# Performance work log

Hardware: AMD Instinct MI355X
Metric: run time of the kernel (lower is better)

Reference implementation:

```python
import jax, jax.numpy as jnp
import numpy as np

B, L = 16384, 200
N_USERS, N_ITEMS, N_CATS, N_DUR = 1_000_000, 100_000, 1000, 50
UD, ID, CD, DD, SD = 64, 64, 16, 8, 64
UDENSE, IDENSE = 25, 3
CONCAT = UD + ID + CD + DD + UDENSE + IDENSE + SD  # 244
NE, EH, EO, NT = 8, 256, 128, 2
T1, T2 = 64, 32  # tower dims
AH1, AH2 = 64, 16  # DIN attention hidden dims
NEG_INF = -1e9


def setup_inputs() -> dict:
    key = jax.random.key(0)
    ks = iter(jax.random.split(key, 40))
    nrm = lambda shape, s: jax.random.normal(next(ks), shape, jnp.float32) * s
    inp = {
        'user_id': jax.random.randint(next(ks), (B,), 0, N_USERS),
        'item_id': jax.random.randint(next(ks), (B,), 0, N_ITEMS),
        'item_category': jax.random.randint(next(ks), (B,), 0, N_CATS),
        'item_dur_bkt': jax.random.randint(next(ks), (B,), 0, N_DUR),
        'user_dense': jax.random.normal(next(ks), (B, UDENSE), jnp.float32),
        'item_dense': jax.random.normal(next(ks), (B, IDENSE), jnp.float32),
        'history_seq': jax.random.randint(next(ks), (B, L), 0, N_ITEMS + 1),
    }
    # embeddings (std=0.01 as in _init_weights); hist row 0 is padding_idx -> zero
    inp['user_E'] = nrm((N_USERS, UD), 0.01)
    inp['item_E'] = nrm((N_ITEMS, ID), 0.01)
    inp['cat_E'] = nrm((N_CATS, CD), 0.01)
    inp['dur_E'] = nrm((N_DUR, DD), 0.01)
    inp['hist_E'] = nrm((N_ITEMS + 1, SD), 0.01).at[0].set(0.0)
    inp['Wproj'] = nrm((ID, SD), 0.12)  # xavier-ish for target_proj (no bias)
    # DIN attention MLP: 4*SD -> 64 -> 16 -> 1
    inp['aW1'] = nrm((4 * SD, AH1), 0.06); inp['ab1'] = jnp.zeros((AH1,), jnp.float32)
    inp['aW2'] = nrm((AH1, AH2), 0.15);    inp['ab2'] = jnp.zeros((AH2,), jnp.float32)
    inp['aW3'] = nrm((AH2, 1), 0.3);       inp['ab3'] = jnp.zeros((1,), jnp.float32)
    # stacked experts: concat -> 256 -> 128 (ReLU both)
    inp['eW1'] = nrm((NE, CONCAT, EH), 0.06); inp['eb1'] = jnp.zeros((NE, EH), jnp.float32)
    inp['eW2'] = nrm((NE, EH, EO), 0.06);     inp['eb2'] = jnp.zeros((NE, EO), jnp.float32)
    # per-task gates: concat -> NE softmax
    inp['gW'] = nrm((NT, CONCAT, NE), 0.06); inp['gb'] = jnp.zeros((NT, NE), jnp.float32)
    # stacked towers: 128 -> 64 -> 32 -> 1
    inp['tW1'] = nrm((NT, EO, T1), 0.09); inp['tb1'] = jnp.zeros((NT, T1), jnp.float32)
    inp['tW2'] = nrm((NT, T1, T2), 0.12); inp['tb2'] = jnp.zeros((NT, T2), jnp.float32)
    inp['tW3'] = nrm((NT, T2, 1), 0.17);  inp['tb3'] = jnp.zeros((NT, 1), jnp.float32)
    return inp


def reference(user_id, item_id, item_category, item_dur_bkt, user_dense, item_dense,
              history_seq, user_E, item_E, cat_E, dur_E, hist_E, Wproj,
              aW1, ab1, aW2, ab2, aW3, ab3,
              eW1, eb1, eW2, eb2, gW, gb,
              tW1, tb1, tW2, tb2, tW3, tb3):
    # --- feature encoding ---
    i_emb = item_E[item_id]            # (B, ID)
    u_emb = user_E[user_id]            # (B, UD)
    c_emb = cat_E[item_category]       # (B, CD)
    d_emb = dur_E[item_dur_bkt]        # (B, DD)
    h_emb = hist_E[history_seq]        # (B, L, SD)
    tgt = (i_emb @ Wproj)[:, None, :]  # (B, 1, SD)
    t = jnp.broadcast_to(tgt, h_emb.shape)
    # DIN attention features: [target, hist, target-hist, target*hist]
    feat = jnp.concatenate([t, h_emb, t - h_emb, t * h_emb], axis=-1)  # (B, L, 4*SD)
    h = jax.nn.relu(feat @ aW1 + ab1)
    h = jax.nn.relu(h @ aW2 + ab2)
    scores = (h @ aW3 + ab3)[..., 0]   # (B, L)
    scores = jnp.where(history_seq == 0, NEG_INF, scores)
    attn = jax.nn.softmax(scores, axis=-1)
    pooled = jnp.einsum('bl,bld->bd', attn, h_emb)  # (B, SD)
    shared = jnp.concatenate([u_emb, i_emb, c_emb, d_emb, user_dense, item_dense, pooled], axis=-1)  # (B, CONCAT)
    # --- experts (batched GEMM) ---
    eh = jax.nn.relu(jnp.einsum('bc,ech->beh', shared, eW1) + eb1)
    eo = jax.nn.relu(jnp.einsum('beh,eho->beo', eh, eW2) + eb2)  # (B, NE, EO)
    # --- per-task gating + towers ---
    gate = jax.nn.softmax(jnp.einsum('bc,tce->bte', shared, gW) + gb, axis=-1)  # (B, T, NE)
    ti = jnp.einsum('bte,beo->bto', gate, eo)  # (B, T, EO)
    x = jax.nn.relu(jnp.einsum('bto,toh->bth', ti, tW1) + tb1)
    x = jax.nn.relu(jnp.einsum('bth,thk->btk', x, tW2) + tb2)
    logit = (jnp.einsum('btk,tkj->btj', x, tW3) + tb3)[..., 0]  # (B, T)
    pred = jax.nn.sigmoid(logit)
    return pred[:, 0], pred[:, 1]
```

## Files before the change

### kernel.cpp

```cpp
#include <hip/hip_runtime.h>
#include <hip/hip_bf16.h>
#include <cstdint>
#include <cmath>


typedef __attribute__((ext_vector_type(8))) short bfrag;
typedef __attribute__((ext_vector_type(4))) float f32x4;

__device__ __forceinline__ unsigned short f2bf(float f) {
  __hip_bfloat16 h = __float2bfloat16(f);
  return __builtin_bit_cast(unsigned short, h);
}
__device__ __forceinline__ float bf2f(unsigned short b) {
  union { unsigned u; float f; } v; v.u = ((unsigned)b) << 16;
  return v.f;
}
__device__ __forceinline__ float bfLo(unsigned hv) {
  union { unsigned u; float f; } v; v.u = hv << 16;
  return v.f;
}
__device__ __forceinline__ float bfHi(unsigned hv) {
  union { unsigned u; float f; } v; v.u = hv & 0xffff0000u;
  return v.f;
}

#define SWZ(row, col) ((col) ^ (((row) & 7) << 3))

static constexpr size_t WS_ATTNB = 0;
static constexpr size_t WS_AW2T  = WS_ATTNB + 16384;
static constexpr size_t WS_A13   = WS_AW2T + 2048;
static constexpr size_t WS_EW1T  = WS_A13 + 16384;
static constexpr size_t WS_EW2T  = WS_EW1T + 1048576;
static constexpr size_t WS_HISTB = WS_EW2T + 524288;
static constexpr size_t WS_TGT   = WS_HISTB + 12800256;
static constexpr size_t WS_TA    = WS_TGT + 2097152;
static constexpr size_t WS_SHP   = WS_TA + 4194304;
static constexpr size_t WS_EO    = WS_SHP + 8388608;
static constexpr size_t WS_GWB   = WS_EO + 33554432;
static constexpr size_t WS_TW1B  = WS_GWB + 8192;
static constexpr size_t WS_TW2B  = WS_TW1B + 32768;
static constexpr size_t WS_WPB   = WS_TW2B + 8192;
static constexpr size_t WS_WAB   = WS_WPB + 8192;

__launch_bounds__(256)
__global__ void k0_prep(const float* __restrict__ aW1, const float* __restrict__ aW2,
                        const float* __restrict__ eW1, const float* __restrict__ eW2,
                        const float* __restrict__ hist_E,
                        const float* __restrict__ gW, const float* __restrict__ tW1,
                        const float* __restrict__ tW2, const float* __restrict__ Wproj,
                        unsigned short* __restrict__ attnBt, unsigned short* __restrict__ aW2t,
                        unsigned short* __restrict__ eW1t, unsigned short* __restrict__ eW2t,
                        unsigned short* __restrict__ hist_b,
                        unsigned short* __restrict__ gWb, unsigned short* __restrict__ tW1b,
                        unsigned short* __restrict__ tW2b,
                        unsigned short* __restrict__ Wpb, unsigned short* __restrict__ WAb) {
  int tid = blockIdx.x * blockDim.x + threadIdx.x;
  int nth = gridDim.x * blockDim.x;
  for (int i = tid; i < 64 * 128; i += nth) {
    int n = i >> 7, k = i & 127;
    float v = (k < 64) ? (aW1[(64 + k) * 64 + n] - aW1[(128 + k) * 64 + n])
                       : aW1[(128 + k) * 64 + n];
    attnBt[i] = f2bf(v);
  }
  for (int i = tid; i < 16 * 64; i += nth) {
    int n = i >> 6, k = i & 63;
    aW2t[i] = f2bf(aW2[k * 16 + n]);
  }
  for (int i = tid; i < 64 * 64; i += nth) {
    int n = i >> 6, k = i & 63;
    Wpb[i] = f2bf(Wproj[k * 64 + n]);
  }
  for (int i = tid; i < 64 * 64; i += nth) {
    int n = i >> 6, k = i & 63;
    float s = 0.f;
    for (int j = 0; j < 64; ++j)
      s += Wproj[k * 64 + j] * (aW1[j * 64 + n] + aW1[(128 + j) * 64 + n]);
    WAb[i] = f2bf(s);
  }
  for (int i = tid; i < 8 * 256 * 256; i += nth) {
    int e = i >> 16, n = (i >> 8) & 255, k = i & 255;
    eW1t[i] = (k < 244) ? f2bf(eW1[(e * 244 + k) * 256 + n]) : (unsigned short)0;
  }
  for (int i = tid; i < 8 * 128 * 256; i += nth) {
    int e = i >> 15, n = (i >> 8) & 127, k = i & 255;
    eW2t[i] = f2bf(eW2[(e * 256 + k) * 128 + n]);
  }
  for (int i = tid; i < 16 * 256; i += nth) {
    int n = i >> 8, k = i & 255, t = n >> 3, e = n & 7;
    gWb[i] = (k < 244) ? f2bf(gW[(t * 244 + k) * 8 + e]) : (unsigned short)0;
  }
  for (int i = tid; i < 2 * 64 * 128; i += nth) {
    int t = i >> 13, n = (i >> 7) & 63, k = i & 127;
    tW1b[i] = f2bf(tW1[(t * 128 + k) * 64 + n]);
  }
  for (int i = tid; i < 2 * 32 * 64; i += nth) {
    int t = i >> 11, n = (i >> 6) & 31, k = i & 63;
    tW2b[i] = f2bf(tW2[(t * 64 + k) * 32 + n]);
  }
  for (int i = tid; i < 100001 * 64; i += nth) hist_b[i] = f2bf(hist_E[i]);
}

__launch_bounds__(256)
__global__ void k1_tgt(const int* __restrict__ item_id, const float* __restrict__ item_E,
                       const unsigned short* __restrict__ Wpb, const unsigned short* __restrict__ WAb,
                       const float* __restrict__ ab1,
                       unsigned short* __restrict__ tgt, float* __restrict__ tA) {
  int tid = threadIdx.x, w = tid >> 6, lane = tid & 63;
  int lr = lane & 15, g = lane >> 4;
  int b0 = blockIdx.x * 64 + w * 16;
  int iid = item_id[b0 + lr];
  bfrag ia[2];
#pragma unroll
  for (int kk = 0; kk < 2; ++kk) {
    const float* src = item_E + (size_t)iid * 64 + kk * 32 + g * 8;
    float4 x = *(const float4*)src;
    float4 y = *(const float4*)(src + 4);
    bfrag r;
    r[0] = (short)f2bf(x.x); r[1] = (short)f2bf(x.y);
    r[2] = (short)f2bf(x.z); r[3] = (short)f2bf(x.w);
    r[4] = (short)f2bf(y.x); r[5] = (short)f2bf(y.y);
    r[6] = (short)f2bf(y.z); r[7] = (short)f2bf(y.w);
    ia[kk] = r;
  }
  f32x4 at[4], aa[4];
#pragma unroll
  for (int i = 0; i < 4; ++i) { at[i] = (f32x4){0,0,0,0}; aa[i] = (f32x4){0,0,0,0}; }
#pragma unroll
  for (int kk = 0; kk < 2; ++kk)
#pragma unroll
    for (int nt = 0; nt < 4; ++nt) {
      bfrag wp = *(const bfrag*)(Wpb + (nt * 16 + lr) * 64 + kk * 32 + g * 8);
      at[nt] = __builtin_amdgcn_mfma_f32_16x16x32_bf16(ia[kk], wp, at[nt], 0, 0, 0);
      bfrag wa = *(const bfrag*)(WAb + (nt * 16 + lr) * 64 + kk * 32 + g * 8);
      aa[nt] = __builtin_amdgcn_mfma_f32_16x16x32_bf16(ia[kk], wa, aa[nt], 0, 0, 0);
    }
#pragma unroll
  for (int nt = 0; nt < 4; ++nt) {
    int n = nt * 16 + lr;
    float b1 = ab1[n];
#pragma unroll
    for (int r = 0; r < 4; ++r) {
      int m = b0 + g * 4 + r;
      tgt[(size_t)m * 64 + n] = f2bf(at[nt][r]);
      tA[(size_t)m * 64 + n] = aa[nt][r] + b1;
    }
  }
}

__launch_bounds__(256)
__global__ void k3a_assemble(const int* __restrict__ user_id, const int* __restrict__ item_id,
                             const int* __restrict__ item_cat, const int* __restrict__ item_dur,
                             const float* __restrict__ user_dense, const float* __restrict__ item_dense,
                             const float* __restrict__ user_E, const float* __restrict__ item_E,
                             const float* __restrict__ cat_E, const float* __restrict__ dur_E,
                             unsigned short* __restrict__ shared_p) {
  int tid = threadIdx.x, w = tid >> 6, lane = tid & 63;
  int b = blockIdx.x * 4 + w;
  unsigned short* row = shared_p + (size_t)b * 256;
  row[lane]      = f2bf(user_E[(size_t)user_id[b] * 64 + lane]);
  row[64 + lane] = f2bf(item_E[(size_t)item_id[b] * 64 + lane]);
  if (lane < 16) row[128 + lane] = f2bf(cat_E[item_cat[b] * 16 + lane]);
  if (lane < 8)  row[144 + lane] = f2bf(dur_E[item_dur[b] * 8 + lane]);
  if (lane < 25) row[152 + lane] = f2bf(user_dense[b * 25 + lane]);
  if (lane < 3)  row[177 + lane] = f2bf(item_dense[b * 3 + lane]);
  if (lane < 12) row[244 + lane] = 0;
}

__launch_bounds__(256, 5)
__global__ void k2_attn(const int* __restrict__ hist_seq, const unsigned short* __restrict__ hist_b,
                        const unsigned short* __restrict__ tgt, const float* __restrict__ tA,
                        const unsigned short* __restrict__ attnBt_g, const unsigned short* __restrict__ aW2t_g,
                        const float* __restrict__ ab2, const float* __restrict__ aW3,
                        unsigned short* __restrict__ shared_p) {
  __shared__ unsigned short sH1[208 * 64];
  __shared__ int   ids[208];
  __shared__ float tv[64], tAv[64];
  __shared__ float sSc[208];
  __shared__ float red[8];
  __shared__ float pbuf[512];
  int b = blockIdx.x;
  int tid = threadIdx.x, w = tid >> 6, lane = tid & 63;
  int lr = lane & 15, g = lane >> 4;

  if (tid < 208) ids[tid] = (tid < 200) ? hist_seq[(size_t)b * 200 + tid] : 0;
  if (tid < 64) tv[tid] = bf2f(tgt[(size_t)b * 64 + tid]);
  else if (tid < 128) tAv[tid - 64] = tA[(size_t)b * 64 + (tid - 64)];

  bfrag b2fr[2];
#pragma unroll
  for (int kk = 0; kk < 2; ++kk)
    b2fr[kk] = *(const bfrag*)(aW2t_g + lr * 64 + kk * 32 + g * 8);
  f32x4 ab2v4 = *(const f32x4*)(ab2 + g * 4);
  f32x4 aW3v4 = *(const f32x4*)(aW3 + g * 4);
  __syncthreads();

  {
    int n = tid >> 2, k0 = (tid & 3) * 16;
    const unsigned short* rowp = attnBt_g + n * 128;
    unsigned short a23[16], a4[16], mo[16];
    *(uint4*)(a23)     = *(const uint4*)(rowp + k0);
    *(uint4*)(a23 + 8) = *(const uint4*)(rowp + k0 + 8);
    *(uint4*)(a4)      = *(const uint4*)(rowp + 64 + k0);
    *(uint4*)(a4 + 8)  = *(const uint4*)(rowp + 64 + k0 + 8);
#pragma unroll
    for (int i = 0; i < 16; ++i)
      mo[i] = f2bf(bf2f(a23[i]) + tv[k0 + i] * bf2f(a4[i]));
    *(uint4*)(sH1 + n * 64 + SWZ(n, k0))     = *(uint4*)(mo);
    *(uint4*)(sH1 + n * 64 + SWZ(n, k0 + 8)) = *(uint4*)(mo + 8);
  }
  __syncthreads();

  bfrag mfr[4][2];
#pragma unroll
  for (int nt = 0; nt < 4; ++nt)
#pragma unroll
    for (int kk = 0; kk < 2; ++kk) {
      int n = nt * 16 + lr;
      mfr[nt][kk] = *(const bfrag*)(sH1 + n * 64 + SWZ(n, kk * 32 + g * 8));
    }
  __syncthreads();

  for (int mt = w; mt < 13; mt += 4) {
    int m = mt * 16 + lr;
    const unsigned short* hrow = hist_b + (size_t)ids[m] * 64;
    bfrag h0 = *(const bfrag*)(hrow + g * 8);
    bfrag h1 = *(const bfrag*)(hrow + 32 + g * 8);
    f32x4 acc[4] = {{0,0,0,0},{0,0,0,0},{0,0,0,0},{0,0,0,0}};
#pragma unroll
    for (int nt = 0; nt < 4; ++nt) {
      acc[nt] = __builtin_amdgcn_mfma_f32_16x16x32_bf16(mfr[nt][0], h0, acc[nt], 0, 0, 0);
      acc[nt] = __builtin_amdgcn_mfma_f32_16x16x32_bf16(mfr[nt][1], h1, acc[nt], 0, 0, 0);
    }
#pragma unroll
    for (int nt = 0; nt < 4; ++nt) {
      f32x4 ta4 = *(const f32x4*)(tAv + nt * 16 + g * 4);
      unsigned lo = (unsigned)f2bf(fmaxf(acc[nt][0] + ta4[0], 0.f))
                  | ((unsigned)f2bf(fmaxf(acc[nt][1] + ta4[1], 0.f)) << 16);
      unsigned hi = (unsigned)f2bf(fmaxf(acc[nt][2] + ta4[2], 0.f))
                  | ((unsigned)f2bf(fmaxf(acc[nt][3] + ta4[3], 0.f)) << 16);
      uint2 pk; pk.x = lo; pk.y = hi;
      *(uint2*)(sH1 + m * 64 + SWZ(m, nt * 16 + g * 4)) = pk;
    }
  }
  __syncthreads();

  for (int mt = w; mt < 13; mt += 4) {
    int m = mt * 16 + lr;
    f32x4 acc2 = {0.f, 0.f, 0.f, 0.f};
#pragma unroll
    for (int kk = 0; kk < 2; ++kk) {
      bfrag hb = *(const bfrag*)(sH1 + m * 64 + SWZ(m, kk * 32 + g * 8));
      acc2 = __builtin_amdgcn_mfma_f32_16x16x32_bf16(b2fr[kk], hb, acc2, 0, 0, 0);
    }
    float p = 0.f;
#pragma unroll
    for (int r = 0; r < 4; ++r)
      p += fmaxf(acc2[r] + ab2v4[r], 0.f) * aW3v4[r];
    p += __shfl_xor(p, 16);
    p += __shfl_xor(p, 32);
    if (lane < 16) sSc[m] = p;
  }
  __syncthreads();

  bool valid = false; float sc0 = 0.f;
  if (tid < 200 && ids[tid] != 0) { valid = true; sc0 = sSc[tid]; }
  float v = valid ? sc0 : -3.0e38f;
#pragma unroll
  for (int d = 1; d < 64; d <<= 1) v = fmaxf(v, __shfl_xor(v, d));
  if (lane == 0) red[w] = v;
  __syncthreads();
  float mx = fmaxf(fmaxf(red[0], red[1]), fmaxf(red[2], red[3]));
  float p = valid ? __expf(sc0 - mx) : 0.f;
  float s = p;
#pragma unroll
  for (int d = 1; d < 64; d <<= 1) s += __shfl_xor(s, d);
  if (lane == 0) red[4 + w] = s;
  if (tid < 208) sSc[tid] = p;
  __syncthreads();
  float denom = red[4] + red[5] + red[6] + red[7] + 1e-30f;

  {
    int hp = lane >> 5, hl = lane & 31;
    float a0 = 0.f, a1 = 0.f;
    for (int i = 0; i < 25; ++i) {
      int l = w * 50 + hp * 25 + i;
      unsigned hv = *(const unsigned*)(hist_b + (size_t)ids[l] * 64 + 2 * hl);
      float pw = sSc[l];
      a0 += pw * bfLo(hv);
      a1 += pw * bfHi(hv);
    }
    pbuf[(w * 2 + hp) * 64 + 2 * hl]     = a0;
    pbuf[(w * 2 + hp) * 64 + 2 * hl + 1] = a1;
  }
  __syncthreads();
  if (tid < 64) {
    float tot = 0.f;
#pragma unroll
    for (int c = 0; c < 8; ++c) tot += pbuf[c * 64 + tid];
    shared_p[(size_t)b * 256 + 180 + tid] = f2bf(tot / denom);
  }
}

__launch_bounds__(256, 2)
__global__ void k3b_experts(const unsigned short* __restrict__ shared_p,
                            const unsigned short* __restrict__ eW1t, const unsigned short* __restrict__ eW2t,
                            const float* __restrict__ eb1, const float* __restrict__ eb2,
                            unsigned short* __restrict__ eo_ws) {
  __shared__ unsigned short sX[64 * 256];
  __shared__ unsigned short sW[256 * 64];
  int tid = threadIdx.x, w = tid >> 6, lane = tid & 63;
  int e = blockIdx.x & 7;
  int b0 = (blockIdx.x >> 3) * 64;
  int lr = lane & 15, g = lane >> 4;

  for (int j = tid; j < 2048; j += 256) {
    int r = j >> 5, ke = (j & 31) * 8;
    uint4 v = *(const uint4*)(shared_p + (size_t)(b0 + r) * 256 + ke);
    *(uint4*)(sX + r * 256 + SWZ(r, ke)) = v;
  }
  f32x4 acc[16];
#pragma unroll
  for (int i = 0; i < 16; ++i) acc[i] = (f32x4){0.f, 0.f, 0.f, 0.f};
  const unsigned short* w1 = eW1t + (size_t)e * 256 * 256;
  for (int c = 0; c < 4; ++c) {
    __syncthreads();
    for (int j = tid; j < 2048; j += 256) {
      int n = j >> 3, ke = (j & 7) * 8;
      uint4 v = *(const uint4*)(w1 + n * 256 + c * 64 + ke);
      *(uint4*)(sW + n * 64 + SWZ(n, ke)) = v;
    }
    __syncthreads();
    int m = w * 16 + lr;
#pragma unroll
    for (int kk = 0; kk < 2; ++kk) {
      int kabs = c * 64 + kk * 32 + g * 8;
      bfrag a = *(const bfrag*)(sX + m * 256 + SWZ(m, kabs));
      int kloc = kk * 32 + g * 8;
#pragma unroll
      for (int nt = 0; nt < 16; ++nt) {
        int n = nt * 16 + lr;
        bfrag bb = *(const bfrag*)(sW + n * 64 + SWZ(n, kloc));
        acc[nt] = __builtin_amdgcn_mfma_f32_16x16x32_bf16(a, bb, acc[nt], 0, 0, 0);
      }
    }
  }
  __syncthreads();
#pragma unroll
  for (int nt = 0; nt < 16; ++nt) {
    int n = nt * 16 + lr;
    float bb = eb1[e * 256 + n];
#pragma unroll
    for (int r = 0; r < 4; ++r) {
      float vv = fmaxf(acc[nt][r] + bb, 0.f);
      int mm = w * 16 + g * 4 + r;
      sX[mm * 256 + SWZ(mm, n)] = f2bf(vv);
    }
  }
  f32x4 acc2[8];
#pragma unroll
  for (int i = 0; i < 8; ++i) acc2[i] = (f32x4){0.f, 0.f, 0.f, 0.f};
  const unsigned short* w2 = eW2t + (size_t)e * 128 * 256;
  for (int c = 0; c < 4; ++c) {
    __syncthreads();
    for (int j = tid; j < 1024; j += 256) {
      int n = j >> 3, ke = (j & 7) * 8;
      uint4 v = *(const uint4*)(w2 + n * 256 + c * 64 + ke);
      *(uint4*)(sW + n * 64 + SWZ(n, ke)) = v;
    }
    __syncthreads();
    int m = w * 16 + lr;
#pragma unroll
    for (int kk = 0; kk < 2; ++kk) {
      int kabs = c * 64 + kk * 32 + g * 8;
      bfrag a = *(const bfrag*)(sX + m * 256 + SWZ(m, kabs));
      int kloc = kk * 32 + g * 8;
#pragma unroll
      for (int nt = 0; nt < 8; ++nt) {
        int n = nt * 16 + lr;
        bfrag bb = *(const bfrag*)(sW + n * 64 + SWZ(n, kloc));
        acc2[nt] = __builtin_amdgcn_mfma_f32_16x16x32_bf16(a, bb, acc2[nt], 0, 0, 0);
      }
    }
  }
#pragma unroll
  for (int nt = 0; nt < 8; ++nt) {
    int n = nt * 16 + lr;
    float bb = eb2[e * 128 + n];
#pragma unroll
    for (int r = 0; r < 4; ++r) {
      float vv = fmaxf(acc2[nt][r] + bb, 0.f);
      int mm = w * 16 + g * 4 + r;
      eo_ws[((size_t)(b0 + mm) * 8 + e) * 128 + n] = f2bf(vv);
    }
  }
}

__launch_bounds__(256, 3)
__global__ void k4_tail(const unsigned short* __restrict__ shared_p, const unsigned short* __restrict__ eo_ws,
                        const unsigned short* __restrict__ gWb, const float* __restrict__ gb,
                        const unsigned short* __restrict__ tW1b, const float* __restrict__ tb1,
                        const unsigned short* __restrict__ tW2b, const float* __restrict__ tb2,
                        const float* __restrict__ tW3, const float* __restrict__ tb3,
                        float* __restrict__ out) {
  __shared__ float sGL[32 * 17];
  __shared__ unsigned short sTi[2 * 32 * 128];
  __shared__ unsigned short sX1[2 * 32 * 64];
  int tid = threadIdx.x, w = tid >> 6, lane = tid & 63;
  int lr = lane & 15, g = lane >> 4;
  int b0 = blockIdx.x * 32;

  if (w < 2) {
    int m = b0 + w * 16 + lr;
    f32x4 acc = {0.f, 0.f, 0.f, 0.f};
#pragma unroll
    for (int kk = 0; kk < 8; ++kk) {
      bfrag a = *(const bfrag*)(shared_p + (size_t)m * 256 + kk * 32 + g * 8);
      bfrag bb = *(const bfrag*)(gWb + lr * 256 + kk * 32 + g * 8);
      acc = __builtin_amdgcn_mfma_f32_16x16x32_bf16(a, bb, acc, 0, 0, 0);
    }
    float gbv = gb[lr];
#pragma unroll
    for (int r = 0; r < 4; ++r)
      sGL[(w * 16 + g * 4 + r) * 17 + lr] = acc[r] + gbv;
  }
  __syncthreads();

  if (tid < 64) {
    int row = tid >> 1, t = tid & 1;
    float* p = sGL + row * 17 + t * 8;
    float mx = -3e38f;
#pragma unroll
    for (int e = 0; e < 8; ++e) mx = fmaxf(mx, p[e]);
    float sum = 0.f; float pe[8];
#pragma unroll
    for (int e = 0; e < 8; ++e) { pe[e] = __expf(p[e] - mx); sum += pe[e]; }
    float inv = 1.f / sum;
#pragma unroll
    for (int e = 0; e < 8; ++e) p[e] = pe[e] * inv;
  }
  __syncthreads();

  {
    int row = tid >> 3, q = tid & 7, t = q >> 2, o0 = (q & 3) * 32;
    const float* gp = sGL + row * 17 + t * 8;
    float accL[16], accH[16];
#pragma unroll
    for (int j = 0; j < 16; ++j) { accL[j] = 0.f; accH[j] = 0.f; }
    const unsigned short* base = eo_ws + ((size_t)(b0 + row) * 8) * 128 + o0;
#pragma unroll
    for (int e = 0; e < 8; ++e) {
      float ge = gp[e];
      const unsigned short* p = base + e * 128;
#pragma unroll
      for (int c = 0; c < 4; ++c) {
        uint4 v = *(const uint4*)(p + c * 8);
        const unsigned* u = (const unsigned*)&v;
#pragma unroll
        for (int j = 0; j < 4; ++j) {
          accL[c * 4 + j] += ge * bfLo(u[j]);
          accH[c * 4 + j] += ge * bfHi(u[j]);
        }
      }
    }
    unsigned short ob[32];
#pragma unroll
    for (int j = 0; j < 16; ++j) {
      ob[2 * j]     = f2bf(accL[j]);
      ob[2 * j + 1] = f2bf(accH[j]);
    }
#pragma unroll
    for (int c = 0; c < 4; ++c)
      *(uint4*)(sTi + t * 4096 + row * 128 + SWZ(row, o0 + c * 8)) = *(const uint4*)(ob + c * 8);
  }
  __syncthreads();

  int t = w >> 1, mt = w & 1;
  {
    f32x4 acc[4] = {{0.f,0.f,0.f,0.f},{0.f,0.f,0.f,0.f},{0.f,0.f,0.f,0.f},{0.f,0.f,0.f,0.f}};
    int ml = mt * 16 + lr;
#pragma unroll
    for (int kk = 0; kk < 4; ++kk) {
      bfrag a = *(const bfrag*)(sTi + t * 4096 + ml * 128 + SWZ(ml, kk * 32 + g * 8));
#pragma unroll
      for (int nt = 0; nt < 4; ++nt) {
        bfrag bb = *(const bfrag*)(tW1b + t * 8192 + (nt * 16 + lr) * 128 + kk * 32 + g * 8);
        acc[nt] = __builtin_amdgcn_mfma_f32_16x16x32_bf16(a, bb, acc[nt], 0, 0, 0);
      }
    }
#pragma unroll
    for (int nt = 0; nt < 4; ++nt) {
      int n = nt * 16 + lr;
      float bias = tb1[t * 64 + n];
#pragma unroll
      for (int r = 0; r < 4; ++r) {
        float x = fmaxf(acc[nt][r] + bias, 0.f);
        int row = mt * 16 + g * 4 + r;
        sX1[t * 2048 + row * 64 + SWZ(row, n)] = f2bf(x);
      }
    }
  }
  __syncthreads();

  {
    f32x4 acc[2] = {{0.f,0.f,0.f,0.f},{0.f,0.f,0.f,0.f}};
    int ml = mt * 16 + lr;
#pragma unroll
    for (int kk = 0; kk < 2; ++kk) {
      bfrag a = *(const bfrag*)(sX1 + t * 2048 + ml * 64 + SWZ(ml, kk * 32 + g * 8));
#pragma unroll
      for (int nt = 0; nt < 2; ++nt) {
        bfrag bb = *(const bfrag*)(tW2b + t * 2048 + (nt * 16 + lr) * 64 + kk * 32 + g * 8);
        acc[nt] = __builtin_amdgcn_mfma_f32_16x16x32_bf16(a, bb, acc[nt], 0, 0, 0);
      }
    }
    float part[4] = {0.f, 0.f, 0.f, 0.f};
#pragma unroll
    for (int nt = 0; nt < 2; ++nt) {
      int n = nt * 16 + lr;
      float bias = tb2[t * 32 + n];
      float w3 = tW3[t * 32 + n];
#pragma unroll
      for (int r = 0; r < 4; ++r)
        part[r] += fmaxf(acc[nt][r] + bias, 0.f) * w3;
    }
#pragma unroll
    for (int d = 1; d < 16; d <<= 1)
#pragma unroll
      for (int r = 0; r < 4; ++r) part[r] += __shfl_xor(part[r], d);
    if (lr == 0) {
      float b3 = tb3[t];
#pragma unroll
      for (int r = 0; r < 4; ++r) {
        float logit = part[r] + b3;
        out[(size_t)t * 16384 + b0 + mt * 16 + g * 4 + r] = 1.f / (1.f + __expf(-logit));
      }
    }
  }
}

extern "C" void kernel_launch(void* const* d_in, const int* in_sizes, int n_in,
                              void* d_out, int out_size, void* d_ws, size_t ws_size,
                              hipStream_t stream) {
  const int*   user_id    = (const int*)  d_in[0];
  const int*   item_id    = (const int*)  d_in[1];
  const int*   item_cat   = (const int*)  d_in[2];
  const int*   item_dur   = (const int*)  d_in[3];
  const float* user_dense = (const float*)d_in[4];
  const float* item_dense = (const float*)d_in[5];
  const int*   hist_seq   = (const int*)  d_in[6];
  const float* user_E     = (const float*)d_in[7];
  const float* item_E     = (const float*)d_in[8];
  const float* cat_E      = (const float*)d_in[9];
  const float* dur_E      = (const float*)d_in[10];
  const float* hist_E     = (const float*)d_in[11];
  const float* Wproj      = (const float*)d_in[12];
  const float* aW1        = (const float*)d_in[13];
  const float* ab1        = (const float*)d_in[14];
  const float* aW2        = (const float*)d_in[15];
  const float* ab2        = (const float*)d_in[16];
  const float* aW3        = (const float*)d_in[17];
  const float* eW1        = (const float*)d_in[19];
  const float* eb1        = (const float*)d_in[20];
  const float* eW2        = (const float*)d_in[21];
  const float* eb2        = (const float*)d_in[22];
  const float* gW         = (const float*)d_in[23];
  const float* gb         = (const float*)d_in[24];
  const float* tW1        = (const float*)d_in[25];
  const float* tb1        = (const float*)d_in[26];
  const float* tW2        = (const float*)d_in[27];
  const float* tb2        = (const float*)d_in[28];
  const float* tW3        = (const float*)d_in[29];
  const float* tb3        = (const float*)d_in[30];
  float* out = (float*)d_out;
  char* ws = (char*)d_ws;

  unsigned short* attnBt  = (unsigned short*)(ws + WS_ATTNB);
  unsigned short* aW2t    = (unsigned short*)(ws + WS_AW2T);
  unsigned short* eW1t    = (unsigned short*)(ws + WS_EW1T);
  unsigned short* eW2t    = (unsigned short*)(ws + WS_EW2T);
  unsigned short* hist_b  = (unsigned short*)(ws + WS_HISTB);
  unsigned short* tgt     = (unsigned short*)(ws + WS_TGT);
  float*          tA      = (float*)         (ws + WS_TA);
  unsigned short* shared_p= (unsigned short*)(ws + WS_SHP);
  unsigned short* eo_ws   = (unsigned short*)(ws + WS_EO);
  unsigned short* gWb     = (unsigned short*)(ws + WS_GWB);
  unsigned short* tW1b    = (unsigned short*)(ws + WS_TW1B);
  unsigned short* tW2b    = (unsigned short*)(ws + WS_TW2B);
  unsigned short* Wpb     = (unsigned short*)(ws + WS_WPB);
  unsigned short* WAb     = (unsigned short*)(ws + WS_WAB);

  k0_prep<<<2048, 256, 0, stream>>>(aW1, aW2, eW1, eW2, hist_E, gW, tW1, tW2, Wproj,
                                    attnBt, aW2t, eW1t, eW2t, hist_b,
                                    gWb, tW1b, tW2b, Wpb, WAb);
  k1_tgt<<<256, 256, 0, stream>>>(item_id, item_E, Wpb, WAb, ab1, tgt, tA);
  k3a_assemble<<<4096, 256, 0, stream>>>(user_id, item_id, item_cat, item_dur,
                                         user_dense, item_dense, user_E, item_E,
                                         cat_E, dur_E, shared_p);
  k2_attn<<<16384, 256, 0, stream>>>(hist_seq, hist_b, tgt, tA, attnBt, aW2t,
                                     ab2, aW3, shared_p);
  k3b_experts<<<2048, 256, 0, stream>>>(shared_p, eW1t, eW2t, eb1, eb2, eo_ws);
  k4_tail<<<512, 256, 0, stream>>>(shared_p, eo_ws, gWb, gb, tW1b, tb1, tW2b, tb2,
                                   tW3, tb3, out);
}
```

Baseline: 244.8 us.

## Reuse MFMA history fragments in registers for attention pooling; vectorize hist conversion

The attention kernel now keeps the history-embedding fragments loaded for the first MFMA in registers and reuses them for the weighted pooling sum, instead of gathering every history row from global memory a second time. The per-thread partial sums go into a padded shared buffer (reusing sH1) and are reduced across lanes and waves at the end. The one-time bf16 conversion of hist_E also moves from scalar to 8-wide vectorized loads and stores. The cost is higher register pressure from holding up to four tiles of fragments plus 16 accumulators, which may hurt occupancy under the 5-blocks launch bound, and a longer final reduction of 64 reads per output.

Result: slower. 335.3 us (+37.0%).

```diff
diff --git a/kernel.cpp b/kernel.cpp
--- a/kernel.cpp
+++ b/kernel.cpp
@@ -97,7 +97,17 @@
     int t = i >> 11, n = (i >> 6) & 31, k = i & 63;
     tW2b[i] = f2bf(tW2[(t * 64 + k) * 32 + n]);
   }
-  for (int i = tid; i < 100001 * 64; i += nth) hist_b[i] = f2bf(hist_E[i]);
+  for (int i = tid; i < 800008; i += nth) {
+    const float* src = hist_E + (size_t)i * 8;
+    float4 a = *(const float4*)src;
+    float4 c = *(const float4*)(src + 4);
+    uint4 q;
+    q.x = (unsigned)f2bf(a.x) | ((unsigned)f2bf(a.y) << 16);
+    q.y = (unsigned)f2bf(a.z) | ((unsigned)f2bf(a.w) << 16);
+    q.z = (unsigned)f2bf(c.x) | ((unsigned)f2bf(c.y) << 16);
+    q.w = (unsigned)f2bf(c.z) | ((unsigned)f2bf(c.w) << 16);
+    *(uint4*)(hist_b + (size_t)i * 8) = q;
+  }
 }
 
 __launch_bounds__(256)
@@ -177,7 +187,6 @@
   __shared__ float tv[64], tAv[64];
   __shared__ float sSc[208];
   __shared__ float red[8];
-  __shared__ float pbuf[512];
   int b = blockIdx.x;
   int tid = threadIdx.x, w = tid >> 6, lane = tid & 63;
   int lr = lane & 15, g = lane >> 4;
@@ -220,45 +229,54 @@
     }
   __syncthreads();
 
-  for (int mt = w; mt < 13; mt += 4) {
-    int m = mt * 16 + lr;
-    const unsigned short* hrow = hist_b + (size_t)ids[m] * 64;
-    bfrag h0 = *(const bfrag*)(hrow + g * 8);
-    bfrag h1 = *(const bfrag*)(hrow + 32 + g * 8);
-    f32x4 acc[4] = {{0,0,0,0},{0,0,0,0},{0,0,0,0},{0,0,0,0}};
-#pragma unroll
-    for (int nt = 0; nt < 4; ++nt) {
-      acc[nt] = __builtin_amdgcn_mfma_f32_16x16x32_bf16(mfr[nt][0], h0, acc[nt], 0, 0, 0);
-      acc[nt] = __builtin_amdgcn_mfma_f32_16x16x32_bf16(mfr[nt][1], h1, acc[nt], 0, 0, 0);
-    }
-#pragma unroll
-    for (int nt = 0; nt < 4; ++nt) {
-      f32x4 ta4 = *(const f32x4*)(tAv + nt * 16 + g * 4);
-      unsigned lo = (unsigned)f2bf(fmaxf(acc[nt][0] + ta4[0], 0.f))
-                  | ((unsigned)f2bf(fmaxf(acc[nt][1] + ta4[1], 0.f)) << 16);
-      unsigned hi = (unsigned)f2bf(fmaxf(acc[nt][2] + ta4[2], 0.f))
-                  | ((unsigned)f2bf(fmaxf(acc[nt][3] + ta4[3], 0.f)) << 16);
-      uint2 pk; pk.x = lo; pk.y = hi;
-      *(uint2*)(sH1 + m * 64 + SWZ(m, nt * 16 + g * 4)) = pk;
-    }
-  }
-  __syncthreads();
-
-  for (int mt = w; mt < 13; mt += 4) {
-    int m = mt * 16 + lr;
-    f32x4 acc2 = {0.f, 0.f, 0.f, 0.f};
-#pragma unroll
-    for (int kk = 0; kk < 2; ++kk) {
-      bfrag hb = *(const bfrag*)(sH1 + m * 64 + SWZ(m, kk * 32 + g * 8));
-      acc2 = __builtin_amdgcn_mfma_f32_16x16x32_bf16(b2fr[kk], hb, acc2, 0, 0, 0);
-    }
-    float p = 0.f;
-#pragma unroll
-    for (int r = 0; r < 4; ++r)
-      p += fmaxf(acc2[r] + ab2v4[r], 0.f) * aW3v4[r];
-    p += __shfl_xor(p, 16);
-    p += __shfl_xor(p, 32);
-    if (lane < 16) sSc[m] = p;
+  bfrag h0s[4], h1s[4];
+#pragma unroll
+  for (int s = 0; s < 4; ++s) {
+    int mt = w + 4 * s;
+    if (mt < 13) {
+      int m = mt * 16 + lr;
+      const unsigned short* hrow = hist_b + (size_t)ids[m] * 64;
+      h0s[s] = *(const bfrag*)(hrow + g * 8);
+      h1s[s] = *(const bfrag*)(hrow + 32 + g * 8);
+      f32x4 acc[4] = {{0,0,0,0},{0,0,0,0},{0,0,0,0},{0,0,0,0}};
+#pragma unroll
+      for (int nt = 0; nt < 4; ++nt) {
+        acc[nt] = __builtin_amdgcn_mfma_f32_16x16x32_bf16(mfr[nt][0], h0s[s], acc[nt], 0, 0, 0);
+        acc[nt] = __builtin_amdgcn_mfma_f32_16x16x32_bf16(mfr[nt][1], h1s[s], acc[nt], 0, 0, 0);
+      }
+#pragma unroll
+      for (int nt = 0; nt < 4; ++nt) {
+        f32x4 ta4 = *(const f32x4*)(tAv + nt * 16 + g * 4);
+        unsigned lo = (unsigned)f2bf(fmaxf(acc[nt][0] + ta4[0], 0.f))
+                    | ((unsigned)f2bf(fmaxf(acc[nt][1] + ta4[1], 0.f)) << 16);
+        unsigned hi = (unsigned)f2bf(fmaxf(acc[nt][2] + ta4[2], 0.f))
+                    | ((unsigned)f2bf(fmaxf(acc[nt][3] + ta4[3], 0.f)) << 16);
+        uint2 pk; pk.x = lo; pk.y = hi;
+        *(uint2*)(sH1 + m * 64 + SWZ(m, nt * 16 + g * 4)) = pk;
+      }
+    }
+  }
+  __syncthreads();
+
+#pragma unroll
+  for (int s = 0; s < 4; ++s) {
+    int mt = w + 4 * s;
+    if (mt < 13) {
+      int m = mt * 16 + lr;
+      f32x4 acc2 = {0.f, 0.f, 0.f, 0.f};
+#pragma unroll
+      for (int kk = 0; kk < 2; ++kk) {
+        bfrag hb = *(const bfrag*)(sH1 + m * 64 + SWZ(m, kk * 32 + g * 8));
+        acc2 = __builtin_amdgcn_mfma_f32_16x16x32_bf16(b2fr[kk], hb, acc2, 0, 0, 0);
+      }
+      float p = 0.f;
+#pragma unroll
+      for (int r = 0; r < 4; ++r)
+        p += fmaxf(acc2[r] + ab2v4[r], 0.f) * aW3v4[r];
+      p += __shfl_xor(p, 16);
+      p += __shfl_xor(p, 32);
+      if (lane < 16) sSc[m] = p;
+    }
   }
   __syncthreads();
 
@@ -277,26 +295,38 @@
   if (lane == 0) red[4 + w] = s;
   if (tid < 208) sSc[tid] = p;
   __syncthreads();
-  float denom = red[4] + red[5] + red[6] + red[7] + 1e-30f;
 
   {
-    int hp = lane >> 5, hl = lane & 31;
-    float a0 = 0.f, a1 = 0.f;
-    for (int i = 0; i < 25; ++i) {
-      int l = w * 50 + hp * 25 + i;
-      unsigned hv = *(const unsigned*)(hist_b + (size_t)ids[l] * 64 + 2 * hl);
-      float pw = sSc[l];
-      a0 += pw * bfLo(hv);
-      a1 += pw * bfHi(hv);
-    }
-    pbuf[(w * 2 + hp) * 64 + 2 * hl]     = a0;
-    pbuf[(w * 2 + hp) * 64 + 2 * hl + 1] = a1;
+    float pacc[16];
+#pragma unroll
+    for (int i = 0; i < 16; ++i) pacc[i] = 0.f;
+#pragma unroll
+    for (int s2 = 0; s2 < 4; ++s2) {
+      int mt = w + 4 * s2;
+      if (mt < 13) {
+        float pm = sSc[mt * 16 + lr];
+#pragma unroll
+        for (int i = 0; i < 8; ++i) {
+          pacc[i]     += pm * bf2f((unsigned short)h0s[s2][i]);
+          pacc[8 + i] += pm * bf2f((unsigned short)h1s[s2][i]);
+        }
+      }
+    }
+    float* sf = (float*)sH1;
+#pragma unroll
+    for (int i = 0; i < 16; ++i) sf[tid * 17 + i] = pacc[i];
   }
   __syncthreads();
   if (tid < 64) {
+    float denom = red[4] + red[5] + red[6] + red[7] + 1e-30f;
+    const float* sf = (const float*)sH1;
+    int d = tid, gg = (d & 31) >> 3, ii = (d & 7) + ((d >> 5) << 3);
     float tot = 0.f;
 #pragma unroll
-    for (int c = 0; c < 8; ++c) tot += pbuf[c * 64 + tid];
+    for (int ww = 0; ww < 4; ++ww)
+#pragma unroll
+      for (int l2 = 0; l2 < 16; ++l2)
+        tot += sf[(ww * 64 + gg * 16 + l2) * 17 + ii];
     shared_p[(size_t)b * 256 + 180 + tid] = f2bf(tot / denom);
   }
 }
```
